# Performance work log

Hardware: AMD Instinct MI355X
Metric: run time of the kernel (lower is better)

Reference implementation:

```python
import jax, jax.numpy as jnp
import numpy as np

DIM = 1024
HEADS = 8
HEAD_DIM = DIM // HEADS
D_STATE = 256
BATCH = 8192
DT_MIN = 1e-3
DT_MAX = 1e-1
EPS = 1e-4  # RMSNorm eps


def setup_inputs() -> dict:
    key = jax.random.key(0)
    ks = jax.random.split(key, 8)
    x_t = jax.random.normal(ks[0], (BATCH, DIM), dtype=jnp.float32)
    state_re = jax.random.normal(ks[1], (BATCH, HEADS, D_STATE), dtype=jnp.float32)
    state_im = jax.random.normal(ks[2], (BATCH, HEADS, D_STATE), dtype=jnp.float32)
    # parameters (match torch init)
    norm_weight = jnp.ones((DIM,), dtype=jnp.float32)
    A_re_log = jnp.full((HEADS, D_STATE), float(np.log(0.5)), dtype=jnp.float32)
    n = jnp.arange(1, D_STATE + 1, dtype=jnp.float32)
    A_im = jnp.broadcast_to(float(np.pi) * n, (HEADS, D_STATE)).astype(jnp.float32)
    b_scale = 1.0 / float(np.sqrt(HEAD_DIM))
    c_scale = 1.0 / float(np.sqrt(D_STATE))
    B_re = jax.random.normal(ks[3], (HEADS, D_STATE, HEAD_DIM), dtype=jnp.float32) * b_scale
    B_im = jax.random.normal(ks[4], (HEADS, D_STATE, HEAD_DIM), dtype=jnp.float32) * b_scale
    C_re = jax.random.normal(ks[5], (HEADS, HEAD_DIM, D_STATE), dtype=jnp.float32) * c_scale
    C_im = jax.random.normal(ks[6], (HEADS, HEAD_DIM, D_STATE), dtype=jnp.float32) * c_scale
    D = jnp.ones((DIM,), dtype=jnp.float32)
    # log_dt: inverse-softplus of log-uniform dt in [dt_min, dt_max]
    u = jax.random.uniform(ks[7], (HEADS, D_STATE), dtype=jnp.float32)
    dt = jnp.exp(u * (np.log(DT_MAX) - np.log(DT_MIN)) + np.log(DT_MIN))
    dt = jnp.maximum(dt, 1e-4)
    log_dt = dt + jnp.log(-jnp.expm1(-dt))
    return dict(x_t=x_t, state_re=state_re, state_im=state_im,
                norm_weight=norm_weight, A_re_log=A_re_log, A_im=A_im,
                B_re=B_re, B_im=B_im, C_re=C_re, C_im=C_im, D=D, log_dt=log_dt)


def reference(x_t, state_re, state_im, norm_weight, A_re_log, A_im,
              B_re, B_im, C_re, C_im, D, log_dt):
    batch = x_t.shape[0]
    # RMSNorm (eps=1e-4, elementwise affine)
    ms = jnp.mean(jnp.square(x_t), axis=-1, keepdims=True)
    x = x_t * jax.lax.rsqrt(ms + EPS) * norm_weight
    x_h = x.reshape(batch, HEADS, HEAD_DIM)  # (B,H,P)
    # discretize
    A = jax.lax.complex(-jnp.exp(A_re_log), A_im)            # (H,N)
    dt = jax.nn.softplus(log_dt)                              # (H,N)
    A_bar = jnp.exp(dt.astype(A.dtype) * A)                   # (H,N) complex
    B = jax.lax.complex(B_re, B_im)                           # (H,N,P)
    C = jax.lax.complex(C_re, C_im)                           # (H,P,N)
    B_bar = ((A_bar - 1.0) / A)[..., None] * B                # (H,N,P)
    # recurrent step
    state = jax.lax.complex(state_re, state_im)               # (B,H,N)
    Bx = jnp.einsum('hnp,bhp->bhn', B_bar, x_h.astype(B_bar.dtype))
    new_state = A_bar[None] * state + Bx                      # (B,H,N)
    Ch = jnp.einsum('hpn,bhn->bhp', C, new_state)             # (B,H,P)
    D_h = D.reshape(HEADS, HEAD_DIM)[None]                    # (1,H,P)
    y_h = 2.0 * Ch.real + D_h * x_h
    out = x_t + y_h.reshape(batch, DIM)
    return out, new_state.real, new_state.imag
```

## Files before the change

kernel.cpp:

```cpp
#include <hip/hip_runtime.h>

#define BATCH 8192
#define DIM 1024
#define HEADS 8
#define HEAD_DIM 128
#define DSTATE 256

typedef __attribute__((ext_vector_type(8))) short short8v;
typedef __attribute__((ext_vector_type(4))) float f32x4;
typedef __attribute__((ext_vector_type(4))) unsigned short ushort4v;
typedef __attribute__((ext_vector_type(4))) unsigned int uint4v;

__device__ __forceinline__ unsigned short f2bf(float x) {
  unsigned int u = __builtin_bit_cast(unsigned int, x);
  unsigned int r = u + 0x7FFFu + ((u >> 16) & 1u);
  return (unsigned short)(r >> 16);
}
__device__ __forceinline__ float bf2f(unsigned short h) {
  unsigned int u = ((unsigned int)h) << 16;
  return __builtin_bit_cast(float, u);
}

__device__ __forceinline__ void stage16f(const float* g, float* l) {
  __builtin_amdgcn_global_load_lds(
      (const __attribute__((address_space(1))) unsigned int*)g,
      (__attribute__((address_space(3))) unsigned int*)l, 16, 0, 0);
}
__device__ __forceinline__ void stage4u(const unsigned short* g, unsigned short* l) {
  __builtin_amdgcn_global_load_lds(
      (const __attribute__((address_space(1))) unsigned int*)g,
      (__attribute__((address_space(3))) unsigned int*)l, 4, 0, 0);
}

#define BARRIER() do { \
  asm volatile("s_waitcnt lgkmcnt(0)" ::: "memory"); \
  __builtin_amdgcn_s_barrier(); \
  asm volatile("" ::: "memory"); } while (0)


__global__ __launch_bounds__(256) void prep(
    const float* __restrict__ logdt, const float* __restrict__ arelog,
    const float* __restrict__ aim,
    const float* __restrict__ Bre, const float* __restrict__ Bim,
    const float* __restrict__ Cre, const float* __restrict__ Cim,
    const float* __restrict__ xtg, const float* __restrict__ normw,
    unsigned short* __restrict__ w1re, unsigned short* __restrict__ w1im,
    unsigned short* __restrict__ w2re, unsigned short* __restrict__ w2mi,
    float* __restrict__ abr, float* __restrict__ abi,
    float* __restrict__ rscale, unsigned short* __restrict__ xhb) {
  const int blk = blockIdx.x;
  if (blk < 1024) {
    const int i = blk * 256 + threadIdx.x;
    const int p = i & 127, s = (i >> 7) & 255, h = i >> 15;
    const int kk = s >> 4, u = s & 15;
    const int n = ((kk >> 1) << 5) + ((u >> 2) & 3) * 8 + (kk & 1) * 4 + (u & 3);
    const int hn = h * 256 + n;
    const float ld = logdt[hn];
    const float dt = log1pf(expf(ld));
    const float Ar = -expf(arelog[hn]);
    const float Ai = aim[hn];
    const float e = expf(dt * Ar), th = dt * Ai;
    const float Abr = e * cosf(th), Abi = e * sinf(th);
    if (p == 0) { abr[h * 256 + s] = Abr; abi[h * 256 + s] = Abi; }
    const float den = Ar * Ar + Ai * Ai;
    const float br_ = Abr - 1.0f;
    const float cr = (br_ * Ar + Abi * Ai) / den;
    const float ci = (Abi * Ar - br_ * Ai) / den;
    const int src = hn * 128 + p;
    const float wb = normw[h * 128 + p];
    const float bre = Bre[src], bim = Bim[src];
    w1re[i] = f2bf((cr * bre - ci * bim) * wb);
    w1im[i] = f2bf((cr * bim + ci * bre) * wb);
  } else if (blk < 2048) {
    const int i = (blk - 1024) * 256 + threadIdx.x;
    w2re[i] = f2bf(Cre[i]);
    w2mi[i] = f2bf(-Cim[i]);
  } else {
    const int wid = threadIdx.x >> 6, lane = threadIdx.x & 63;
    const int row = (blk - 2048) * 4 + wid;
    const float* xr = xtg + (size_t)row * DIM;
    unsigned short* xo = xhb + (size_t)row * DIM;
    f32x4 v[4];
    float ssq = 0.f;
    #pragma unroll
    for (int c = 0; c < 4; ++c) {
      v[c] = *(const f32x4*)(xr + c * 256 + lane * 4);
      ssq += v[c][0]*v[c][0] + v[c][1]*v[c][1] + v[c][2]*v[c][2] + v[c][3]*v[c][3];
    }
    #pragma unroll
    for (int m = 1; m < 64; m <<= 1) ssq += __shfl_xor(ssq, m, 64);
    const float sc = rsqrtf(ssq * (1.0f / DIM) + 1e-4f);
    if (lane == 0) rscale[row] = 1.0f / sc;
    #pragma unroll
    for (int c = 0; c < 4; ++c) {
      ushort4v o;
      o[0] = f2bf(v[c][0] * sc); o[1] = f2bf(v[c][1] * sc);
      o[2] = f2bf(v[c][2] * sc); o[3] = f2bf(v[c][3] * sc);
      *(ushort4v*)(xo + c * 256 + lane * 4) = o;
    }
  }
}

__global__ __launch_bounds__(512, 2) void s5_main(
    const unsigned short* __restrict__ w1re, const unsigned short* __restrict__ w1im,
    const unsigned short* __restrict__ w2re, const unsigned short* __restrict__ w2mi,
    const float* __restrict__ abrp, const float* __restrict__ abip,
    const float* __restrict__ rscale, const unsigned short* __restrict__ xhb,
    const float* __restrict__ sre, const float* __restrict__ sim,
    const float* __restrict__ dvec, const float* __restrict__ normw,
    float* __restrict__ out, float* __restrict__ nsre, float* __restrict__ nsim) {
  __shared__ float Sb[3][2][16][256];
  __shared__ unsigned short xbL[3][16][128];
  __shared__ unsigned short pf[2][8][64][8];
  __shared__ float rsL[256];
  const int tid = threadIdx.x;
  const int w = tid >> 6, lane = tid & 63;
  const int g = lane >> 4, bl = lane & 15;
  const int h = blockIdx.x & 7;
  const int blkrow = (blockIdx.x >> 3) * 256;

  short8v w1r[2][4], w1i[2][4];
  #pragma unroll
  for (int t = 0; t < 2; ++t) {
    const int kk = 2 * w + t;
    const unsigned short* pr = w1re + ((size_t)(h * DSTATE + kk * 16 + bl)) * HEAD_DIM + g * 8;
    const unsigned short* pi = w1im + ((size_t)(h * DSTATE + kk * 16 + bl)) * HEAD_DIM + g * 8;
    #pragma unroll
    for (int ks = 0; ks < 4; ++ks) {
      w1r[t][ks] = *(const short8v*)(pr + ks * 32);
      w1i[t][ks] = *(const short8v*)(pi + ks * 32);
    }
  }
  short8v w2r[8], w2i[8];
  {
    const unsigned short* qr = w2re + ((size_t)(h * HEAD_DIM + w * 16 + bl)) * DSTATE + g * 8;
    const unsigned short* qi = w2mi + ((size_t)(h * HEAD_DIM + w * 16 + bl)) * DSTATE + g * 8;
    #pragma unroll
    for (int j = 0; j < 8; ++j) {
      w2r[j] = *(const short8v*)(qr + j * 32);
      w2i[j] = *(const short8v*)(qi + j * 32);
    }
  }
  f32x4 Arh[2], Aih[2];
  #pragma unroll
  for (int t = 0; t < 2; ++t) {
    Arh[t] = *(const f32x4*)(abrp + h * DSTATE + (2 * w + t) * 16 + g * 4);
    Aih[t] = *(const f32x4*)(abip + h * DSTATE + (2 * w + t) * 16 + g * 4);
  }
  f32x4 d4;
  {
    const int col = h * HEAD_DIM + w * 16 + g * 4;
    const f32x4 dv = *(const f32x4*)(dvec + col);
    const f32x4 nv = *(const f32x4*)(normw + col);
    #pragma unroll
    for (int r = 0; r < 4; ++r) d4[r] = dv[r] * nv[r];
  }
  const int srcA = ((g >> 1) << 4) + bl;
  const int srcB = (((g >> 1) + 2) << 4) + bl;

  auto STAGE = [&](int t) {
    const int b = t % 3;
    const int gr0 = blkrow + t * 16;
    #pragma unroll
    for (int i = 0; i < 2; ++i) {
      const int row = 2 * w + i;
      const size_t rb = ((size_t)(gr0 + row) * HEADS + h) * DSTATE;
      const int soff = (lane ^ (row & 7)) * 4;
      stage16f(sre + rb + soff, &Sb[b][0][row][0]);
      stage16f(sim + rb + soff, &Sb[b][1][row][0]);
    }
    #pragma unroll
    for (int i = 0; i < 2; ++i) {
      const int row = 2 * w + i;
      const unsigned short* src = xhb + (size_t)(gr0 + row) * DIM + h * HEAD_DIM
          + (((lane >> 2) ^ (row & 7)) << 3) + ((lane & 3) << 1);
      stage4u(src, &xbL[b][row][0]);
    }
  };

  auto PHASE1 = [&](int t) {
    const int b = t % 3;
    short8v xf[4];
    #pragma unroll
    for (int ks = 0; ks < 4; ++ks)
      xf[ks] = *(const short8v*)&xbL[b][bl][(((ks * 4 + g) ^ (bl & 7)) << 3)];
    f32x4 nre[2], nim[2];
    unsigned pr0 = 0, pr1 = 0, pi0 = 0, pi1 = 0;
    #pragma unroll
    for (int tt = 0; tt < 2; ++tt) {
      f32x4 dr = {0.f,0.f,0.f,0.f};
      f32x4 di = {0.f,0.f,0.f,0.f};
      #pragma unroll
      for (int ks = 0; ks < 4; ++ks)
        dr = __builtin_amdgcn_mfma_f32_16x16x32_bf16(w1r[tt][ks], xf[ks], dr, 0, 0, 0);
      #pragma unroll
      for (int ks = 0; ks < 4; ++ks)
        di = __builtin_amdgcn_mfma_f32_16x16x32_bf16(w1i[tt][ks], xf[ks], di, 0, 0, 0);
      const int c = (((8 * w + 2 * g + tt) ^ (bl & 7)) << 2);
      const f32x4 s_r = *(const f32x4*)&Sb[b][0][bl][c];
      const f32x4 s_i = *(const f32x4*)&Sb[b][1][bl][c];
      f32x4 nr, ni;
      #pragma unroll
      for (int r = 0; r < 4; ++r) {
        nr[r] = fmaf(Arh[tt][r], s_r[r], fmaf(-Aih[tt][r], s_i[r], dr[r]));
        ni[r] = fmaf(Arh[tt][r], s_i[r], fmaf(Aih[tt][r], s_r[r], di[r]));
      }
      nre[tt] = nr; nim[tt] = ni;
      unsigned lo  = (unsigned)f2bf(nr[0]) | ((unsigned)f2bf(nr[1]) << 16);
      unsigned hi  = (unsigned)f2bf(nr[2]) | ((unsigned)f2bf(nr[3]) << 16);
      unsigned lo2 = (unsigned)f2bf(ni[0]) | ((unsigned)f2bf(ni[1]) << 16);
      unsigned hi2 = (unsigned)f2bf(ni[2]) | ((unsigned)f2bf(ni[3]) << 16);
      if (tt == 0) { pr0 = lo; pr1 = hi; pi0 = lo2; pi1 = hi2; }
      else {
        uint4v urv; urv[0] = pr0; urv[1] = pr1; urv[2] = lo;  urv[3] = hi;
        uint4v uiv; uiv[0] = pi0; uiv[1] = pi1; uiv[2] = lo2; uiv[3] = hi2;
        *(short8v*)&pf[0][w][lane][0] = __builtin_bit_cast(short8v, urv);
        *(short8v*)&pf[1][w][lane][0] = __builtin_bit_cast(short8v, uiv);
      }
    }
    f32x4 v1r, v2r, v1i, v2i;
    #pragma unroll
    for (int e = 0; e < 4; ++e) {
      float a1 = __shfl(nre[0][e], srcA, 64);
      float b1 = __shfl(nre[1][e], srcA, 64);
      v1r[e] = (g & 1) ? b1 : a1;
      float a2 = __shfl(nre[0][e], srcB, 64);
      float b2 = __shfl(nre[1][e], srcB, 64);
      v2r[e] = (g & 1) ? b2 : a2;
      float c1 = __shfl(nim[0][e], srcA, 64);
      float d1 = __shfl(nim[1][e], srcA, 64);
      v1i[e] = (g & 1) ? d1 : c1;
      float c2 = __shfl(nim[0][e], srcB, 64);
      float d2 = __shfl(nim[1][e], srcB, 64);
      v2i[e] = (g & 1) ? d2 : c2;
    }
    const size_t no = ((size_t)(blkrow + t * 16 + bl) * HEADS + h) * DSTATE + w * 32 + g * 4;
    *(f32x4*)(nsre + no)      = v1r;
    *(f32x4*)(nsre + no + 16) = v2r;
    *(f32x4*)(nsim + no)      = v1i;
    *(f32x4*)(nsim + no + 16) = v2i;
  };

  auto PHASE2 = [&](int t) {
    const int b = t % 3;
    f32x4 a2 = {0.f,0.f,0.f,0.f};
    #pragma unroll
    for (int j = 0; j < 8; ++j) {
      const short8v pbr = *(const short8v*)&pf[0][j][lane][0];
      const short8v pbi = *(const short8v*)&pf[1][j][lane][0];
      a2 = __builtin_amdgcn_mfma_f32_16x16x32_bf16(w2r[j], pbr, a2, 0, 0, 0);
      a2 = __builtin_amdgcn_mfma_f32_16x16x32_bf16(w2i[j], pbi, a2, 0, 0, 0);
    }
    const float rs = rsL[t * 16 + bl];
    const int col = h * HEAD_DIM + w * 16 + g * 4;
    const size_t o = (size_t)(blkrow + t * 16 + bl) * DIM + col;
    const unsigned short* xp =
        &xbL[b][bl][(((2 * w + (g >> 1)) ^ (bl & 7)) << 3) + ((g & 1) << 2)];
    f32x4 ro;
    #pragma unroll
    for (int r = 0; r < 4; ++r)
      ro[r] = bf2f(xp[r]) * (rs + d4[r]) + 2.0f * a2[r];
    *(f32x4*)(out + o) = ro;
  };

  if (w == 0) stage16f(rscale + blkrow + lane * 4, &rsL[0]);
  STAGE(0);
  STAGE(1);

  for (int t = 0; t < 16; ++t) {
    if (t == 0)       asm volatile("s_waitcnt vmcnt(6)"  ::: "memory");
    else if (t == 1)  asm volatile("s_waitcnt vmcnt(11)" ::: "memory");
    else if (t <= 14) asm volatile("s_waitcnt vmcnt(16)" ::: "memory");
    else              asm volatile("s_waitcnt vmcnt(10)" ::: "memory");
    BARRIER();
    if (t + 2 < 16) STAGE(t + 2);
    __builtin_amdgcn_sched_barrier(0);
    PHASE1(t);
    BARRIER();
    PHASE2(t);
  }
}

extern "C" void kernel_launch(void* const* d_in, const int* in_sizes, int n_in,
                              void* d_out, int out_size, void* d_ws, size_t ws_size,
                              hipStream_t stream) {
  const float* x_t      = (const float*)d_in[0];
  const float* state_re = (const float*)d_in[1];
  const float* state_im = (const float*)d_in[2];
  const float* norm_w   = (const float*)d_in[3];
  const float* A_re_log = (const float*)d_in[4];
  const float* A_im     = (const float*)d_in[5];
  const float* B_re     = (const float*)d_in[6];
  const float* B_im     = (const float*)d_in[7];
  const float* C_re     = (const float*)d_in[8];
  const float* C_im     = (const float*)d_in[9];
  const float* Dv       = (const float*)d_in[10];
  const float* log_dt   = (const float*)d_in[11];

  float* out   = (float*)d_out;
  float* ns_re = out + (size_t)BATCH * DIM;
  float* ns_im = ns_re + (size_t)BATCH * HEADS * DSTATE;

  char* ws = (char*)d_ws;
  unsigned short* w1re = (unsigned short*)ws;
  unsigned short* w1im = w1re + 262144;
  unsigned short* w2re = w1im + 262144;
  unsigned short* w2mi = w2re + 262144;
  float* abr    = (float*)(ws + 4 * 524288);
  float* abi    = abr + 2048;
  float* rscale = abi + 2048;
  unsigned short* xhb = (unsigned short*)(rscale + 8192);

  prep<<<4096, 256, 0, stream>>>(log_dt, A_re_log, A_im, B_re, B_im, C_re, C_im,
                                 x_t, norm_w, w1re, w1im, w2re, w2mi,
                                 abr, abi, rscale, xhb);
  s5_main<<<256, 512, 0, stream>>>(w1re, w1im, w2re, w2mi, abr, abi, rscale, xhb,
                                   state_re, state_im, Dv, norm_w,
                                   out, ns_re, ns_im);
}
```

Baseline: 91.25 us.

## Fuse weight discretization into main kernel and split PHASE2 MFMA accumulator chain

Moves the B_bar/C bf16 weight preparation and A_bar computation out of the prep kernel and into each s5_main workgroup's prologue, computing them straight from fp32 parameters into registers. The first state/x staging loads are issued before this prologue so the transcendental and conversion work overlaps the initial global loads. This removes the workspace round trip for the weights and shrinks the prep grid. In exchange, every one of the 256 blocks redoes the discretization math and reads fp32 B/C (twice the bytes). PHASE2 also uses two independent MFMA accumulators to shorten the dependency chain.

```diff
diff --git a/kernel.cpp b/kernel.cpp
--- a/kernel.cpp
+++ b/kernel.cpp
@@ -20,6 +20,14 @@
   unsigned int u = ((unsigned int)h) << 16;
   return __builtin_bit_cast(float, u);
 }
+__device__ __forceinline__ short8v pack8(const f32x4 a, const f32x4 b) {
+  uint4v u;
+  u[0] = (unsigned)f2bf(a[0]) | ((unsigned)f2bf(a[1]) << 16);
+  u[1] = (unsigned)f2bf(a[2]) | ((unsigned)f2bf(a[3]) << 16);
+  u[2] = (unsigned)f2bf(b[0]) | ((unsigned)f2bf(b[1]) << 16);
+  u[3] = (unsigned)f2bf(b[2]) | ((unsigned)f2bf(b[3]) << 16);
+  return __builtin_bit_cast(short8v, u);
+}
 
 __device__ __forceinline__ void stage16f(const float* g, float* l) {
   __builtin_amdgcn_global_load_lds(
@@ -39,72 +47,37 @@
 
 
 __global__ __launch_bounds__(256) void prep(
+    const float* __restrict__ xtg,
+    float* __restrict__ rscale, unsigned short* __restrict__ xhb) {
+  const int wid = threadIdx.x >> 6, lane = threadIdx.x & 63;
+  const int row = blockIdx.x * 4 + wid;
+  const float* xr = xtg + (size_t)row * DIM;
+  unsigned short* xo = xhb + (size_t)row * DIM;
+  f32x4 v[4];
+  float ssq = 0.f;
+  #pragma unroll
+  for (int c = 0; c < 4; ++c) {
+    v[c] = *(const f32x4*)(xr + c * 256 + lane * 4);
+    ssq += v[c][0]*v[c][0] + v[c][1]*v[c][1] + v[c][2]*v[c][2] + v[c][3]*v[c][3];
+  }
+  #pragma unroll
+  for (int m = 1; m < 64; m <<= 1) ssq += __shfl_xor(ssq, m, 64);
+  const float sc = rsqrtf(ssq * (1.0f / DIM) + 1e-4f);
+  if (lane == 0) rscale[row] = 1.0f / sc;
+  #pragma unroll
+  for (int c = 0; c < 4; ++c) {
+    ushort4v o;
+    o[0] = f2bf(v[c][0] * sc); o[1] = f2bf(v[c][1] * sc);
+    o[2] = f2bf(v[c][2] * sc); o[3] = f2bf(v[c][3] * sc);
+    *(ushort4v*)(xo + c * 256 + lane * 4) = o;
+  }
+}
+
+__global__ __launch_bounds__(512, 2) void s5_main(
     const float* __restrict__ logdt, const float* __restrict__ arelog,
     const float* __restrict__ aim,
     const float* __restrict__ Bre, const float* __restrict__ Bim,
     const float* __restrict__ Cre, const float* __restrict__ Cim,
-    const float* __restrict__ xtg, const float* __restrict__ normw,
-    unsigned short* __restrict__ w1re, unsigned short* __restrict__ w1im,
-    unsigned short* __restrict__ w2re, unsigned short* __restrict__ w2mi,
-    float* __restrict__ abr, float* __restrict__ abi,
-    float* __restrict__ rscale, unsigned short* __restrict__ xhb) {
-  const int blk = blockIdx.x;
-  if (blk < 1024) {
-    const int i = blk * 256 + threadIdx.x;
-    const int p = i & 127, s = (i >> 7) & 255, h = i >> 15;
-    const int kk = s >> 4, u = s & 15;
-    const int n = ((kk >> 1) << 5) + ((u >> 2) & 3) * 8 + (kk & 1) * 4 + (u & 3);
-    const int hn = h * 256 + n;
-    const float ld = logdt[hn];
-    const float dt = log1pf(expf(ld));
-    const float Ar = -expf(arelog[hn]);
-    const float Ai = aim[hn];
-    const float e = expf(dt * Ar), th = dt * Ai;
-    const float Abr = e * cosf(th), Abi = e * sinf(th);
-    if (p == 0) { abr[h * 256 + s] = Abr; abi[h * 256 + s] = Abi; }
-    const float den = Ar * Ar + Ai * Ai;
-    const float br_ = Abr - 1.0f;
-    const float cr = (br_ * Ar + Abi * Ai) / den;
-    const float ci = (Abi * Ar - br_ * Ai) / den;
-    const int src = hn * 128 + p;
-    const float wb = normw[h * 128 + p];
-    const float bre = Bre[src], bim = Bim[src];
-    w1re[i] = f2bf((cr * bre - ci * bim) * wb);
-    w1im[i] = f2bf((cr * bim + ci * bre) * wb);
-  } else if (blk < 2048) {
-    const int i = (blk - 1024) * 256 + threadIdx.x;
-    w2re[i] = f2bf(Cre[i]);
-    w2mi[i] = f2bf(-Cim[i]);
-  } else {
-    const int wid = threadIdx.x >> 6, lane = threadIdx.x & 63;
-    const int row = (blk - 2048) * 4 + wid;
-    const float* xr = xtg + (size_t)row * DIM;
-    unsigned short* xo = xhb + (size_t)row * DIM;
-    f32x4 v[4];
-    float ssq = 0.f;
-    #pragma unroll
-    for (int c = 0; c < 4; ++c) {
-      v[c] = *(const f32x4*)(xr + c * 256 + lane * 4);
-      ssq += v[c][0]*v[c][0] + v[c][1]*v[c][1] + v[c][2]*v[c][2] + v[c][3]*v[c][3];
-    }
-    #pragma unroll
-    for (int m = 1; m < 64; m <<= 1) ssq += __shfl_xor(ssq, m, 64);
-    const float sc = rsqrtf(ssq * (1.0f / DIM) + 1e-4f);
-    if (lane == 0) rscale[row] = 1.0f / sc;
-    #pragma unroll
-    for (int c = 0; c < 4; ++c) {
-      ushort4v o;
-      o[0] = f2bf(v[c][0] * sc); o[1] = f2bf(v[c][1] * sc);
-      o[2] = f2bf(v[c][2] * sc); o[3] = f2bf(v[c][3] * sc);
-      *(ushort4v*)(xo + c * 256 + lane * 4) = o;
-    }
-  }
-}
-
-__global__ __launch_bounds__(512, 2) void s5_main(
-    const unsigned short* __restrict__ w1re, const unsigned short* __restrict__ w1im,
-    const unsigned short* __restrict__ w2re, const unsigned short* __restrict__ w2mi,
-    const float* __restrict__ abrp, const float* __restrict__ abip,
     const float* __restrict__ rscale, const unsigned short* __restrict__ xhb,
     const float* __restrict__ sre, const float* __restrict__ sim,
     const float* __restrict__ dvec, const float* __restrict__ normw,
@@ -119,45 +92,6 @@
   const int h = blockIdx.x & 7;
   const int blkrow = (blockIdx.x >> 3) * 256;
 
-  short8v w1r[2][4], w1i[2][4];
-  #pragma unroll
-  for (int t = 0; t < 2; ++t) {
-    const int kk = 2 * w + t;
-    const unsigned short* pr = w1re + ((size_t)(h * DSTATE + kk * 16 + bl)) * HEAD_DIM + g * 8;
-    const unsigned short* pi = w1im + ((size_t)(h * DSTATE + kk * 16 + bl)) * HEAD_DIM + g * 8;
-    #pragma unroll
-    for (int ks = 0; ks < 4; ++ks) {
-      w1r[t][ks] = *(const short8v*)(pr + ks * 32);
-      w1i[t][ks] = *(const short8v*)(pi + ks * 32);
-    }
-  }
-  short8v w2r[8], w2i[8];
-  {
-    const unsigned short* qr = w2re + ((size_t)(h * HEAD_DIM + w * 16 + bl)) * DSTATE + g * 8;
-    const unsigned short* qi = w2mi + ((size_t)(h * HEAD_DIM + w * 16 + bl)) * DSTATE + g * 8;
-    #pragma unroll
-    for (int j = 0; j < 8; ++j) {
-      w2r[j] = *(const short8v*)(qr + j * 32);
-      w2i[j] = *(const short8v*)(qi + j * 32);
-    }
-  }
-  f32x4 Arh[2], Aih[2];
-  #pragma unroll
-  for (int t = 0; t < 2; ++t) {
-    Arh[t] = *(const f32x4*)(abrp + h * DSTATE + (2 * w + t) * 16 + g * 4);
-    Aih[t] = *(const f32x4*)(abip + h * DSTATE + (2 * w + t) * 16 + g * 4);
-  }
-  f32x4 d4;
-  {
-    const int col = h * HEAD_DIM + w * 16 + g * 4;
-    const f32x4 dv = *(const f32x4*)(dvec + col);
-    const f32x4 nv = *(const f32x4*)(normw + col);
-    #pragma unroll
-    for (int r = 0; r < 4; ++r) d4[r] = dv[r] * nv[r];
-  }
-  const int srcA = ((g >> 1) << 4) + bl;
-  const int srcB = (((g >> 1) + 2) << 4) + bl;
-
   auto STAGE = [&](int t) {
     const int b = t % 3;
     const int gr0 = blkrow + t * 16;
@@ -177,6 +111,89 @@
       stage4u(src, &xbL[b][row][0]);
     }
   };
+
+  if (w == 0) stage16f(rscale + blkrow + lane * 4, &rsL[0]);
+  STAGE(0);
+  STAGE(1);
+
+  short8v w1r[2][4], w1i[2][4];
+  #pragma unroll
+  for (int tt = 0; tt < 2; ++tt) {
+    const int n = 32 * w + ((bl >> 2) & 3) * 8 + tt * 4 + (bl & 3);
+    const int hn = h * 256 + n;
+    const float ld = logdt[hn];
+    const float dtv = log1pf(expf(ld));
+    const float Ar = -expf(arelog[hn]);
+    const float Ai = aim[hn];
+    const float ee = expf(dtv * Ar), th = dtv * Ai;
+    const float Abr = ee * cosf(th), Abi = ee * sinf(th);
+    const float den = Ar * Ar + Ai * Ai;
+    const float br_ = Abr - 1.0f;
+    const float cr = (br_ * Ar + Abi * Ai) / den;
+    const float ci = (Abi * Ar - br_ * Ai) / den;
+    #pragma unroll
+    for (int ks = 0; ks < 4; ++ks) {
+      const size_t po = (size_t)hn * 128 + ks * 32 + g * 8;
+      const f32x4 br0 = *(const f32x4*)(Bre + po);
+      const f32x4 br1 = *(const f32x4*)(Bre + po + 4);
+      const f32x4 bi0 = *(const f32x4*)(Bim + po);
+      const f32x4 bi1 = *(const f32x4*)(Bim + po + 4);
+      const int nwo = h * 128 + ks * 32 + g * 8;
+      const f32x4 nw0 = *(const f32x4*)(normw + nwo);
+      const f32x4 nw1 = *(const f32x4*)(normw + nwo + 4);
+      f32x4 r0, r1, i0, i1;
+      #pragma unroll
+      for (int r = 0; r < 4; ++r) {
+        r0[r] = (cr * br0[r] - ci * bi0[r]) * nw0[r];
+        i0[r] = (cr * bi0[r] + ci * br0[r]) * nw0[r];
+        r1[r] = (cr * br1[r] - ci * bi1[r]) * nw1[r];
+        i1[r] = (cr * bi1[r] + ci * br1[r]) * nw1[r];
+      }
+      w1r[tt][ks] = pack8(r0, r1);
+      w1i[tt][ks] = pack8(i0, i1);
+    }
+  }
+  short8v w2r[8], w2i[8];
+  #pragma unroll
+  for (int j = 0; j < 8; ++j) {
+    const size_t co = ((size_t)(h * 128 + w * 16 + bl)) * 256 + j * 32 + g * 8;
+    const f32x4 c0 = *(const f32x4*)(Cre + co);
+    const f32x4 c1 = *(const f32x4*)(Cre + co + 4);
+    const f32x4 d0 = *(const f32x4*)(Cim + co);
+    const f32x4 d1 = *(const f32x4*)(Cim + co + 4);
+    f32x4 m0, m1;
+    #pragma unroll
+    for (int r = 0; r < 4; ++r) { m0[r] = -d0[r]; m1[r] = -d1[r]; }
+    w2r[j] = pack8(c0, c1);
+    w2i[j] = pack8(m0, m1);
+  }
+  f32x4 Arh[2], Aih[2];
+  #pragma unroll
+  for (int tt = 0; tt < 2; ++tt) {
+    const int nb = h * 256 + 32 * w + 8 * g + 4 * tt;
+    const f32x4 ld4 = *(const f32x4*)(logdt + nb);
+    const f32x4 ar4 = *(const f32x4*)(arelog + nb);
+    const f32x4 ai4 = *(const f32x4*)(aim + nb);
+    #pragma unroll
+    for (int r = 0; r < 4; ++r) {
+      const float dtv = log1pf(expf(ld4[r]));
+      const float Ar = -expf(ar4[r]);
+      const float Ai = ai4[r];
+      const float ee = expf(dtv * Ar), th = dtv * Ai;
+      Arh[tt][r] = ee * cosf(th);
+      Aih[tt][r] = ee * sinf(th);
+    }
+  }
+  f32x4 d4;
+  {
+    const int col = h * HEAD_DIM + w * 16 + g * 4;
+    const f32x4 dv = *(const f32x4*)(dvec + col);
+    const f32x4 nv = *(const f32x4*)(normw + col);
+    #pragma unroll
+    for (int r = 0; r < 4; ++r) d4[r] = dv[r] * nv[r];
+  }
+  const int srcA = ((g >> 1) << 4) + bl;
+  const int srcB = (((g >> 1) + 2) << 4) + bl;
 
   auto PHASE1 = [&](int t) {
     const int b = t % 3;
@@ -244,12 +261,18 @@
   auto PHASE2 = [&](int t) {
     const int b = t % 3;
     f32x4 a2 = {0.f,0.f,0.f,0.f};
-    #pragma unroll
-    for (int j = 0; j < 8; ++j) {
-      const short8v pbr = *(const short8v*)&pf[0][j][lane][0];
-      const short8v pbi = *(const short8v*)&pf[1][j][lane][0];
-      a2 = __builtin_amdgcn_mfma_f32_16x16x32_bf16(w2r[j], pbr, a2, 0, 0, 0);
-      a2 = __builtin_amdgcn_mfma_f32_16x16x32_bf16(w2i[j], pbi, a2, 0, 0, 0);
+    f32x4 a2b = {0.f,0.f,0.f,0.f};
+    #pragma unroll
+    for (int jj = 0; jj < 4; ++jj) {
+      const int j0 = 2 * jj, j1 = 2 * jj + 1;
+      const short8v pbr0 = *(const short8v*)&pf[0][j0][lane][0];
+      const short8v pbi0 = *(const short8v*)&pf[1][j0][lane][0];
+      const short8v pbr1 = *(const short8v*)&pf[0][j1][lane][0];
+      const short8v pbi1 = *(const short8v*)&pf[1][j1][lane][0];
+      a2  = __builtin_amdgcn_mfma_f32_16x16x32_bf16(w2r[j0], pbr0, a2, 0, 0, 0);
+      a2b = __builtin_amdgcn_mfma_f32_16x16x32_bf16(w2r[j1], pbr1, a2b, 0, 0, 0);
+      a2  = __builtin_amdgcn_mfma_f32_16x16x32_bf16(w2i[j0], pbi0, a2, 0, 0, 0);
+      a2b = __builtin_amdgcn_mfma_f32_16x16x32_bf16(w2i[j1], pbi1, a2b, 0, 0, 0);
     }
     const float rs = rsL[t * 16 + bl];
     const int col = h * HEAD_DIM + w * 16 + g * 4;
@@ -259,13 +282,9 @@
     f32x4 ro;
     #pragma unroll
     for (int r = 0; r < 4; ++r)
-      ro[r] = bf2f(xp[r]) * (rs + d4[r]) + 2.0f * a2[r];
+      ro[r] = bf2f(xp[r]) * (rs + d4[r]) + 2.0f * (a2[r] + a2b[r]);
     *(f32x4*)(out + o) = ro;
   };
-
-  if (w == 0) stage16f(rscale + blkrow + lane * 4, &rsL[0]);
-  STAGE(0);
-  STAGE(1);
 
   for (int t = 0; t < 16; ++t) {
     if (t == 0)       asm volatile("s_waitcnt vmcnt(6)"  ::: "memory");
@@ -302,19 +321,11 @@
   float* ns_im = ns_re + (size_t)BATCH * HEADS * DSTATE;
 
   char* ws = (char*)d_ws;
-  unsigned short* w1re = (unsigned short*)ws;
-  unsigned short* w1im = w1re + 262144;
-  unsigned short* w2re = w1im + 262144;
-  unsigned short* w2mi = w2re + 262144;
-  float* abr    = (float*)(ws + 4 * 524288);
-  float* abi    = abr + 2048;
-  float* rscale = abi + 2048;
+  float* rscale = (float*)ws;
   unsigned short* xhb = (unsigned short*)(rscale + 8192);
 
-  prep<<<4096, 256, 0, stream>>>(log_dt, A_re_log, A_im, B_re, B_im, C_re, C_im,
-                                 x_t, norm_w, w1re, w1im, w2re, w2mi,
-                                 abr, abi, rscale, xhb);
-  s5_main<<<256, 512, 0, stream>>>(w1re, w1im, w2re, w2mi, abr, abi, rscale, xhb,
-                                   state_re, state_im, Dv, norm_w,
+  prep<<<2048, 256, 0, stream>>>(x_t, rscale, xhb);
+  s5_main<<<256, 512, 0, stream>>>(log_dt, A_re_log, A_im, B_re, B_im, C_re, C_im,
+                                   rscale, xhb, state_re, state_im, Dv, norm_w,
                                    out, ns_re, ns_im);
 }
```

Result: slower. 138.1 us (+51.3%).
